# Kernel tuning notes

Measured on AMD Instinct MI355X. Metric: run time of the kernel, lower is better.

Reference implementation:

```python
import jax, jax.numpy as jnp
import numpy as np
import math

N, KZ, IFZ, AHZ, AFZ = 20000, 16, 256, 8, 32
EPS = 1e-5


def layernorm(x, g, b):
    m = jnp.mean(x, axis=-1, keepdims=True)
    v = jnp.mean((x - m) ** 2, axis=-1, keepdims=True)
    return (x - m) * jax.lax.rsqrt(v + EPS) * g + b


def rotate_half(x):
    x1, x2 = jnp.split(x, 2, axis=-1)
    return jnp.concatenate([-x2, x1], axis=-1)


def setup_inputs() -> dict:
    key = jax.random.key(0)
    ks = jax.random.split(key, 16)
    s = 1.0 / math.sqrt(IFZ)
    hf = AHZ * AFZ
    return {
        "x_1": jax.random.normal(ks[0], (N, IFZ), jnp.float32),
        "x_2": jax.random.normal(ks[1], (N, KZ, IFZ), jnp.float32),
        "pos_emb": jax.random.normal(ks[2], (N, AFZ), jnp.float32),
        "edge_index": jax.random.randint(ks[3], (N, KZ), 0, N),
        "Wq": jax.random.normal(ks[4], (IFZ, hf), jnp.float32) * s,
        "Wk": jax.random.normal(ks[5], (IFZ, hf), jnp.float32) * s,
        "Wv": jax.random.normal(ks[6], (IFZ, hf), jnp.float32) * s,
        "Wb": jax.random.normal(ks[7], (IFZ, AHZ), jnp.float32) * s,
        "bln_g": jnp.ones((IFZ,), jnp.float32),
        "bln_b": jnp.zeros((IFZ,), jnp.float32),
        "Wg": jax.random.normal(ks[8], (IFZ, hf), jnp.float32) * s,
        "bg": jnp.zeros((hf,), jnp.float32),
        "Wback": jax.random.normal(ks[9], (hf, IFZ), jnp.float32) / math.sqrt(hf),
        "bback": jnp.zeros((IFZ,), jnp.float32),
        "ln1_g": jnp.ones((IFZ,), jnp.float32),
        "ln1_b": jnp.zeros((IFZ,), jnp.float32),
    }


def reference(x_1, x_2, pos_emb, edge_index, Wq, Wk, Wv, Wb, bln_g, bln_b,
              Wg, bg, Wback, bback, ln1_g, ln1_b):
    n = x_1.shape[0]
    y_1 = x_1[edge_index]                                  # [N,kz,ifz] irregular gather
    q = (x_1 @ Wq).reshape(n, AHZ, AFZ)                    # [N,h,f]
    k = (y_1 @ Wk).reshape(n, KZ, AHZ, AFZ)                # [N,kz,h,f]
    # RoPE: rotate q by each node's own angles, k by gathered neighbor angles
    cos_q = jnp.cos(pos_emb)[:, None, :]                   # [N,1,f]
    sin_q = jnp.sin(pos_emb)[:, None, :]
    q = q * cos_q + rotate_half(q) * sin_q
    pe_n = pos_emb[edge_index]                             # [N,kz,f]
    cos_k = jnp.cos(pe_n)[:, :, None, :]                   # [N,kz,1,f]
    sin_k = jnp.sin(pe_n)[:, :, None, :]
    k = k * cos_k + rotate_half(k) * sin_k
    v = (y_1 @ Wv).reshape(n, KZ, AHZ, AFZ)
    bias_2 = layernorm(x_2, bln_g, bln_b) @ Wb             # [N,kz,h]
    gate = jax.nn.sigmoid(x_1 @ Wg + bg).reshape(n, AHZ, AFZ)
    scores = jnp.einsum('nhf,nkhf->nkh', q, k) / math.sqrt(AFZ) + bias_2
    w = jax.nn.softmax(scores, axis=1)                     # over kz neighbors
    out = gate * jnp.einsum('nkh,nkhf->nhf', w, v)         # [N,h,f]
    out = out.reshape(n, AHZ * AFZ) @ Wback + bback + math.sqrt(2.0) * x_1
    return layernorm(out, ln1_g, ln1_b)
```

## Files before the change

### kernel.cpp

```cpp
#include <hip/hip_runtime.h>
#include <math.h>

#define IFZ 256
#define KZ  16
#define AHZ 8
#define AFZ 32
#define HF  256

typedef _Float16 half8 __attribute__((ext_vector_type(8)));
typedef _Float16 half4 __attribute__((ext_vector_type(4)));
typedef float    f32x4 __attribute__((ext_vector_type(4)));

__global__ void prep_all(const float* __restrict__ w0, const float* __restrict__ w1,
                         const float* __restrict__ w2, const float* __restrict__ w3,
                         const float* __restrict__ w4, _Float16* __restrict__ out,
                         const float* __restrict__ g, const float* __restrict__ b,
                         const float* __restrict__ Wb,
                         _Float16* __restrict__ c1T, float* __restrict__ c23)
{
    const int m = blockIdx.y;
    if (m < 5) {
        int k = blockIdx.x;
        int c = threadIdx.x;
        const float* w = (m == 0) ? w0 : (m == 1) ? w1 : (m == 2) ? w2 : (m == 3) ? w3 : w4;
        out[(size_t)m * 65536 + (size_t)c * 256 + k] = (_Float16)w[(size_t)k * 256 + c];
        return;
    }
    if (blockIdx.x != 0) return;

    __shared__ float red[4][16];
    const int f = threadIdx.x;
    const int w = f >> 6, l = f & 63;
    const float gv = g[f], bv = b[f];
    float ph2[8], ph3[8];
    #pragma unroll
    for (int h = 0; h < 8; ++h) {
        float wv = Wb[(size_t)f * 8 + h];
        c1T[h * 256 + f] = (_Float16)(gv * wv);
        ph2[h] = gv * wv;
        ph3[h] = bv * wv;
    }
    c1T[8 * 256 + f] = (_Float16)1.0f;
    #pragma unroll
    for (int cc = 9; cc < 16; ++cc) c1T[cc * 256 + f] = (_Float16)0.0f;

    #pragma unroll
    for (int h = 0; h < 8; ++h) {
        #pragma unroll
        for (int o = 32; o > 0; o >>= 1) {
            ph2[h] += __shfl_xor(ph2[h], o);
            ph3[h] += __shfl_xor(ph3[h], o);
        }
        if (l == h) { red[w][h] = ph2[h]; red[w][8 + h] = ph3[h]; }
    }
    __syncthreads();
    if (f < 16) c23[f] = red[0][f] + red[1][f] + red[2][f] + red[3][f];
}

__launch_bounds__(256)
__global__ void gemm_qkvg(const float* __restrict__ A, const _Float16* __restrict__ WT,
                          const float* __restrict__ pe, const float* __restrict__ bg,
                          _Float16* __restrict__ QH, _Float16* __restrict__ KH,
                          _Float16* __restrict__ VH, _Float16* __restrict__ GH, int N)
{
    __shared__ _Float16 as[64][40];
    __shared__ _Float16 bs[4][64][40];

    const int tid = threadIdx.x;
    const int l   = tid & 63;
    const int w   = tid >> 6;
    const int n0  = blockIdx.x * 64;
    const int c0  = blockIdx.y * 64;

    f32x4 acc[4][4];
    #pragma unroll
    for (int m = 0; m < 4; ++m)
        #pragma unroll
        for (int b = 0; b < 4; ++b)
            { acc[m][b][0]=0.f; acc[m][b][1]=0.f; acc[m][b][2]=0.f; acc[m][b][3]=0.f; }

    const int srow = tid >> 2;
    const int sch  = (tid & 3) * 8;
    const size_t aoff = (size_t)(n0 + srow) * IFZ + sch;
    const size_t boff = (size_t)(c0 + srow) * IFZ + sch;
    const bool arow_ok = (n0 + srow < N);

    half8 av{}, bv0, bv1, bv2, bv3;
    if (arow_ok) {
        f32x4 a0 = *reinterpret_cast<const f32x4*>(A + aoff);
        f32x4 a1 = *reinterpret_cast<const f32x4*>(A + aoff + 4);
        av[0]=(_Float16)a0[0]; av[1]=(_Float16)a0[1]; av[2]=(_Float16)a0[2]; av[3]=(_Float16)a0[3];
        av[4]=(_Float16)a1[0]; av[5]=(_Float16)a1[1]; av[6]=(_Float16)a1[2]; av[7]=(_Float16)a1[3];
    }
    bv0 = *reinterpret_cast<const half8*>(WT + 0 * 65536 + boff);
    bv1 = *reinterpret_cast<const half8*>(WT + 1 * 65536 + boff);
    bv2 = *reinterpret_cast<const half8*>(WT + 2 * 65536 + boff);
    bv3 = *reinterpret_cast<const half8*>(WT + 3 * 65536 + boff);

    for (int kt = 0; kt < 8; ++kt) {
        __syncthreads();
        *reinterpret_cast<half8*>(&as[srow][sch])    = av;
        *reinterpret_cast<half8*>(&bs[0][srow][sch]) = bv0;
        *reinterpret_cast<half8*>(&bs[1][srow][sch]) = bv1;
        *reinterpret_cast<half8*>(&bs[2][srow][sch]) = bv2;
        *reinterpret_cast<half8*>(&bs[3][srow][sch]) = bv3;
        __syncthreads();

        half8 nav{}, nbv0{}, nbv1{}, nbv2{}, nbv3{};
        if (kt < 7) {
            const int k0 = (kt + 1) * 32;
            if (arow_ok) {
                f32x4 a0 = *reinterpret_cast<const f32x4*>(A + aoff + k0);
                f32x4 a1 = *reinterpret_cast<const f32x4*>(A + aoff + k0 + 4);
                nav[0]=(_Float16)a0[0]; nav[1]=(_Float16)a0[1]; nav[2]=(_Float16)a0[2]; nav[3]=(_Float16)a0[3];
                nav[4]=(_Float16)a1[0]; nav[5]=(_Float16)a1[1]; nav[6]=(_Float16)a1[2]; nav[7]=(_Float16)a1[3];
            }
            nbv0 = *reinterpret_cast<const half8*>(WT + 0 * 65536 + boff + k0);
            nbv1 = *reinterpret_cast<const half8*>(WT + 1 * 65536 + boff + k0);
            nbv2 = *reinterpret_cast<const half8*>(WT + 2 * 65536 + boff + k0);
            nbv3 = *reinterpret_cast<const half8*>(WT + 3 * 65536 + boff + k0);
        }

        half8 af = *reinterpret_cast<const half8*>(&as[16 * w + (l & 15)][8 * (l >> 4)]);
        #pragma unroll
        for (int m = 0; m < 4; ++m) {
            #pragma unroll
            for (int b = 0; b < 4; ++b) {
                half8 bf = *reinterpret_cast<const half8*>(&bs[m][16 * b + (l & 15)][8 * (l >> 4)]);
                acc[m][b] = __builtin_amdgcn_mfma_f32_16x16x32_f16(af, bf, acc[m][b], 0, 0, 0);
            }
        }
        av = nav; bv0 = nbv0; bv1 = nbv1; bv2 = nbv2; bv3 = nbv3;
    }

    #pragma unroll
    for (int r = 0; r < 4; ++r) {
        const int grow = n0 + 16 * w + ((l >> 4) << 2) + r;
        if (grow >= N) continue;
        float a0 = pe[(size_t)grow * AFZ + (l & 15)];
        float a1 = pe[(size_t)grow * AFZ + 16 + (l & 15)];
        float s0, c0f, s1, c1f;
        __sincosf(a0, &s0, &c0f);
        __sincosf(a1, &s1, &c1f);
        #pragma unroll
        for (int m = 0; m < 2; ++m) {
            _Float16* o = m ? KH : QH;
            #pragma unroll
            for (int pb = 0; pb < 4; pb += 2) {
                float v0 = acc[m][pb][r], v1 = acc[m][pb + 1][r];
                o[(size_t)grow * HF + c0 + 16 * pb       + (l & 15)] = (_Float16)(v0 * c0f - v1 * s0);
                o[(size_t)grow * HF + c0 + 16 * (pb + 1) + (l & 15)] = (_Float16)(v1 * c1f + v0 * s1);
            }
        }
        #pragma unroll
        for (int b = 0; b < 4; ++b)
            VH[(size_t)grow * HF + c0 + 16 * b + (l & 15)] = (_Float16)acc[2][b][r];
        #pragma unroll
        for (int b = 0; b < 4; ++b) {
            const int c = c0 + 16 * b + (l & 15);
            float v = acc[3][b][r] + bg[c];
            GH[(size_t)grow * HF + c] = (_Float16)(1.f / (1.f + __expf(-v)));
        }
    }
}

__launch_bounds__(256)
__global__ void attn_fused(const _Float16* __restrict__ Qh, const _Float16* __restrict__ Kh,
                           const _Float16* __restrict__ Vh, const _Float16* __restrict__ Gh,
                           const int* __restrict__ eidx, const float* __restrict__ x2,
                           const _Float16* __restrict__ c1T, const float* __restrict__ c23,
                           _Float16* __restrict__ AOh, int N)
{
    const int tid = threadIdx.x;
    const int l   = tid & 63;
    const int w   = tid >> 6;
    const int n   = blockIdx.x * 4 + w;
    if (n >= N) return;
    const int h = l >> 3;
    const int c = l & 15;
    const int p = l >> 4;

    const int ei_reg = eidx[(size_t)n * KZ + c];

    const float* xr = x2 + ((size_t)n * KZ + c) * IFZ + p * 8;
    f32x4 xv[16];
    #pragma unroll
    for (int kt = 0; kt < 8; ++kt) {
        xv[2 * kt]     = __builtin_nontemporal_load(reinterpret_cast<const f32x4*>(xr + kt * 32));
        xv[2 * kt + 1] = __builtin_nontemporal_load(reinterpret_cast<const f32x4*>(xr + kt * 32 + 4));
    }
    half8 bf[8];
    #pragma unroll
    for (int kt = 0; kt < 8; ++kt)
        bf[kt] = *reinterpret_cast<const half8*>(c1T + (size_t)c * 256 + kt * 32 + p * 8);

    f32x4 acc1 = {0.f, 0.f, 0.f, 0.f};
    f32x4 acc2 = {0.f, 0.f, 0.f, 0.f};
    #pragma unroll
    for (int kt = 0; kt < 8; ++kt) {
        f32x4 xa = xv[2 * kt], xb = xv[2 * kt + 1];
        half8 ax, ax2;
        ax[0] = (_Float16)xa[0]; ax[1] = (_Float16)xa[1];
        ax[2] = (_Float16)xa[2]; ax[3] = (_Float16)xa[3];
        ax[4] = (_Float16)xb[0]; ax[5] = (_Float16)xb[1];
        ax[6] = (_Float16)xb[2]; ax[7] = (_Float16)xb[3];
        ax2[0] = (_Float16)(xa[0] * xa[0]); ax2[1] = (_Float16)(xa[1] * xa[1]);
        ax2[2] = (_Float16)(xa[2] * xa[2]); ax2[3] = (_Float16)(xa[3] * xa[3]);
        ax2[4] = (_Float16)(xb[0] * xb[0]); ax2[5] = (_Float16)(xb[1] * xb[1]);
        ax2[6] = (_Float16)(xb[2] * xb[2]); ax2[7] = (_Float16)(xb[3] * xb[3]);
        acc1 = __builtin_amdgcn_mfma_f32_16x16x32_f16(ax,  bf[kt], acc1, 0, 0, 0);
        acc2 = __builtin_amdgcn_mfma_f32_16x16x32_f16(ax2, bf[kt], acc2, 0, 0, 0);
    }

    const float c2v = (c < 8) ? c23[c]     : 0.f;
    const float c3v = (c < 8) ? c23[8 + c] : 0.f;
    const int srcl = (l & 48) | 8;
    float bval[4];
    #pragma unroll
    for (int j = 0; j < 4; ++j) {
        float s1 = __shfl(acc1[j], srcl);
        float s2 = __shfl(acc2[j], srcl);
        float m    = s1 * (1.f / 256.f);
        float var  = s2 * (1.f / 256.f) - m * m;
        float rstd = rsqrtf(var + 1e-5f);
        bval[j] = rstd * (acc1[j] - m * c2v) + c3v;
    }

    half4 kreg[16];
    #pragma unroll
    for (int e = 0; e < 16; ++e) {
        const int row = __shfl(ei_reg, e);
        kreg[e] = *reinterpret_cast<const half4*>(Kh + (size_t)row * HF + 4 * l);
    }
    half4 vreg[16];
    #pragma unroll
    for (int e = 0; e < 16; ++e) {
        const int row = __shfl(ei_reg, e);
        vreg[e] = *reinterpret_cast<const half4*>(Vh + (size_t)row * HF + 4 * l);
    }

    half4 qh4 = *reinterpret_cast<const half4*>(Qh + (size_t)n * HF + 4 * l);
    const float q0 = (float)qh4[0], q1 = (float)qh4[1],
                q2 = (float)qh4[2], q3 = (float)qh4[3];

    float sc[16];
    #pragma unroll
    for (int e = 0; e < 16; ++e) {
        float s = q0 * (float)kreg[e][0] + q1 * (float)kreg[e][1]
                + q2 * (float)kreg[e][2] + q3 * (float)kreg[e][3];
        s += __shfl_xor(s, 1); s += __shfl_xor(s, 2); s += __shfl_xor(s, 4);
        sc[e] = s * 0.17677669529663687f
              + __shfl(bval[e & 3], ((e >> 2) << 4) | h);
    }

    float m = sc[0];
    #pragma unroll
    for (int e = 1; e < 16; ++e) m = fmaxf(m, sc[e]);
    float sum = 0.f;
    #pragma unroll
    for (int e = 0; e < 16; ++e) { sc[e] = __expf(sc[e] - m); sum += sc[e]; }
    const float inv = 1.f / sum;

    float o0 = 0.f, o1 = 0.f, o2 = 0.f, o3 = 0.f;
    #pragma unroll
    for (int e = 0; e < 16; ++e) {
        const float we = sc[e] * inv;
        o0 = fmaf(we, (float)vreg[e][0], o0);
        o1 = fmaf(we, (float)vreg[e][1], o1);
        o2 = fmaf(we, (float)vreg[e][2], o2);
        o3 = fmaf(we, (float)vreg[e][3], o3);
    }

    half4 gh4 = *reinterpret_cast<const half4*>(Gh + (size_t)n * HF + 4 * l);
    half4 oh;
    oh[0] = (_Float16)(o0 * (float)gh4[0]);
    oh[1] = (_Float16)(o1 * (float)gh4[1]);
    oh[2] = (_Float16)(o2 * (float)gh4[2]);
    oh[3] = (_Float16)(o3 * (float)gh4[3]);
    *reinterpret_cast<half4*>(AOh + (size_t)n * HF + 4 * l) = oh;
}

__launch_bounds__(256)
__global__ void gemm_back(const _Float16* __restrict__ A, const _Float16* __restrict__ BT,
                          const float* __restrict__ bias, float* __restrict__ Y, int N)
{
    __shared__ _Float16 as[64][40];
    __shared__ _Float16 bs[64][40];

    const int tid = threadIdx.x;
    const int l   = tid & 63;
    const int w   = tid >> 6;
    const int n0  = blockIdx.x * 64;
    const int c0  = blockIdx.y * 64;

    f32x4 acc[4];
    #pragma unroll
    for (int b = 0; b < 4; ++b) { acc[b][0]=0.f; acc[b][1]=0.f; acc[b][2]=0.f; acc[b][3]=0.f; }

    const int srow = tid >> 2;
    const int sch  = (tid & 3) * 8;
    const size_t aoff = (size_t)(n0 + srow) * IFZ + sch;
    const size_t boff = (size_t)(c0 + srow) * IFZ + sch;

    half8 av{}, bv;
    if (n0 + srow < N) av = *reinterpret_cast<const half8*>(A + aoff);
    bv = *reinterpret_cast<const half8*>(BT + boff);

    for (int kt = 0; kt < 8; ++kt) {
        __syncthreads();
        *reinterpret_cast<half8*>(&as[srow][sch]) = av;
        *reinterpret_cast<half8*>(&bs[srow][sch]) = bv;
        __syncthreads();

        half8 nav{}, nbv{};
        if (kt < 7) {
            const int k0 = (kt + 1) * 32;
            if (n0 + srow < N) nav = *reinterpret_cast<const half8*>(A + aoff + k0);
            nbv = *reinterpret_cast<const half8*>(BT + boff + k0);
        }

        half8 af = *reinterpret_cast<const half8*>(&as[16 * w + (l & 15)][8 * (l >> 4)]);
        #pragma unroll
        for (int b = 0; b < 4; ++b) {
            half8 bf = *reinterpret_cast<const half8*>(&bs[16 * b + (l & 15)][8 * (l >> 4)]);
            acc[b] = __builtin_amdgcn_mfma_f32_16x16x32_f16(af, bf, acc[b], 0, 0, 0);
        }
        av = nav; bv = nbv;
    }

    #pragma unroll
    for (int r = 0; r < 4; ++r) {
        const int grow = n0 + 16 * w + ((l >> 4) << 2) + r;
        if (grow >= N) continue;
        #pragma unroll
        for (int b = 0; b < 4; ++b) {
            const int c = c0 + 16 * b + (l & 15);
            Y[(size_t)grow * HF + c] = acc[b][r] + bias[c];
        }
    }
}

__launch_bounds__(256)
__global__ void final_ln(const float* __restrict__ RAWb,
                         const float* __restrict__ x1b,
                         const float* __restrict__ g1,
                         const float* __restrict__ b1,
                         float* __restrict__ outb,
                         int N)
{
    int n    = blockIdx.x * 4 + (threadIdx.x >> 6);
    int lane = threadIdx.x & 63;
    if (n >= N) return;
    const size_t off = (size_t)n * IFZ + lane * 4;
    float4 ur = *reinterpret_cast<const float4*>(RAWb + off);
    float4 ux = *reinterpret_cast<const float4*>(x1b + off);
    float x[4];
    x[0] = ur.x + 1.4142135623730951f * ux.x;
    x[1] = ur.y + 1.4142135623730951f * ux.y;
    x[2] = ur.z + 1.4142135623730951f * ux.z;
    x[3] = ur.w + 1.4142135623730951f * ux.w;
    float s = x[0] + x[1] + x[2] + x[3];
    float q = x[0]*x[0] + x[1]*x[1] + x[2]*x[2] + x[3]*x[3];
    #pragma unroll
    for (int o = 32; o > 0; o >>= 1) { s += __shfl_xor(s, o); q += __shfl_xor(q, o); }
    float m    = s * (1.f / 256.f);
    float var  = q * (1.f / 256.f) - m * m;
    float rstd = rsqrtf(var + 1e-5f);
    float4 uo;
    {
        int f = lane * 4;
        uo.x = (x[0] - m) * rstd * g1[f + 0] + b1[f + 0];
        uo.y = (x[1] - m) * rstd * g1[f + 1] + b1[f + 1];
        uo.z = (x[2] - m) * rstd * g1[f + 2] + b1[f + 2];
        uo.w = (x[3] - m) * rstd * g1[f + 3] + b1[f + 3];
    }
    *reinterpret_cast<float4*>(outb + off) = uo;
}

extern "C" void kernel_launch(void* const* d_in, const int* in_sizes, int n_in,
                              void* d_out, int out_size, void* d_ws, size_t ws_size,
                              hipStream_t stream)
{
    const float* x1   = (const float*)d_in[0];
    const float* x2   = (const float*)d_in[1];
    const float* pe   = (const float*)d_in[2];
    const int*   ei   = (const int*)d_in[3];
    const float* wq   = (const float*)d_in[4];
    const float* wk   = (const float*)d_in[5];
    const float* wv   = (const float*)d_in[6];
    const float* wb   = (const float*)d_in[7];
    const float* blng = (const float*)d_in[8];
    const float* blnb = (const float*)d_in[9];
    const float* wg   = (const float*)d_in[10];
    const float* bg   = (const float*)d_in[11];
    const float* wbk  = (const float*)d_in[12];
    const float* bbk  = (const float*)d_in[13];
    const float* g1   = (const float*)d_in[14];
    const float* b1   = (const float*)d_in[15];

    const int N = in_sizes[0] / IFZ;

    const size_t S2 = (((size_t)N * HF * 2) + 4095) & ~(size_t)4095;
    char* base = (char*)d_ws;
    _Float16* QH  = (_Float16*)(base);
    _Float16* KH  = (_Float16*)(base + 1 * S2);
    _Float16* VH  = (_Float16*)(base + 2 * S2);
    _Float16* GH  = (_Float16*)(base + 3 * S2);
    _Float16* WT  = (_Float16*)(base + 4 * S2);
    _Float16* C1T = (_Float16*)(base + 4 * S2 + (1u << 20));
    float*    C23 = (float*)   (base + 4 * S2 + (1u << 20) + 8192);
    _Float16* AOH = QH;
    float*    RAW = (float*)(base + 1 * S2);

    prep_all<<<dim3(256, 6), 256, 0, stream>>>(wq, wk, wv, wg, wbk, WT,
                                               blng, blnb, wb, C1T, C23);

    const int nt = (N + 63) / 64;
    gemm_qkvg<<<dim3(nt, 4), 256, 0, stream>>>(x1, WT, pe, bg, QH, KH, VH, GH, N);

    attn_fused<<<dim3((N + 3) / 4), 256, 0, stream>>>(QH, KH, VH, GH, ei, x2,
                                                      C1T, C23, AOH, N);

    gemm_back<<<dim3(nt, 4), 256, 0, stream>>>(AOH, WT + 4 * 65536, bbk, RAW, N);

    final_ln<<<dim3((N + 3) / 4), 256, 0, stream>>>(RAW, x1, g1, b1, (float*)d_out, N);
}
```

Measured before the change: 171.2 us.

## Move x_2 layernorm bias computation into QKVG GEMM launch as interleaved blocks

The streaming layernorm-bias computation over x_2 moves out of the attention kernel and into the QKVG GEMM launch as extra blocks, interleaved with the GEMM tiles through a proportional block mapping. The bias results go to a new B2 workspace buffer that the attention kernel reads back. This lets the bandwidth-heavy x_2 read overlap with the compute-bound GEMM and makes the attention kernel lighter. The cost is an extra write and read of an N*16*8 float buffer, plus a more complex block dispatch.

```diff
diff --git a/kernel.cpp b/kernel.cpp
--- a/kernel.cpp
+++ b/kernel.cpp
@@ -58,19 +58,85 @@
 }
 
 __launch_bounds__(256)
-__global__ void gemm_qkvg(const float* __restrict__ A, const _Float16* __restrict__ WT,
-                          const float* __restrict__ pe, const float* __restrict__ bg,
-                          _Float16* __restrict__ QH, _Float16* __restrict__ KH,
-                          _Float16* __restrict__ VH, _Float16* __restrict__ GH, int N)
+__global__ void qkvg_bias2(const float* __restrict__ A, const _Float16* __restrict__ WT,
+                           const float* __restrict__ pe, const float* __restrict__ bg,
+                           _Float16* __restrict__ QH, _Float16* __restrict__ KH,
+                           _Float16* __restrict__ VH, _Float16* __restrict__ GH,
+                           const float* __restrict__ x2, const _Float16* __restrict__ c1T,
+                           const float* __restrict__ c23, float* __restrict__ B2,
+                           int N, int R, int Aq, int grid)
 {
     __shared__ _Float16 as[64][40];
     __shared__ _Float16 bs[4][64][40];
+
+    const int bx  = blockIdx.x;
+    const long long t0 = (long long)bx * Aq / grid;
+    const long long t1 = (long long)(bx + 1) * Aq / grid;
+    const bool is_q = (t1 > t0);
 
     const int tid = threadIdx.x;
     const int l   = tid & 63;
     const int w   = tid >> 6;
-    const int n0  = blockIdx.x * 64;
-    const int c0  = blockIdx.y * 64;
+
+    if (!is_q) {
+        const int bidx = bx - (int)t0;
+        const int c = l & 15;
+        const int p = l >> 4;
+        const int R0 = (bidx * 4 + w) * 16;
+        if (R0 >= R) return;
+
+        const int arow = (R0 + c < R) ? (R0 + c) : (R - 1);
+        const float* xr = x2 + (size_t)arow * IFZ + p * 8;
+
+        f32x4 xv[16];
+        #pragma unroll
+        for (int kt = 0; kt < 8; ++kt) {
+            xv[2 * kt]     = __builtin_nontemporal_load(reinterpret_cast<const f32x4*>(xr + kt * 32));
+            xv[2 * kt + 1] = __builtin_nontemporal_load(reinterpret_cast<const f32x4*>(xr + kt * 32 + 4));
+        }
+        half8 bf[8];
+        #pragma unroll
+        for (int kt = 0; kt < 8; ++kt)
+            bf[kt] = *reinterpret_cast<const half8*>(c1T + (size_t)c * 256 + kt * 32 + p * 8);
+
+        f32x4 acc1 = {0.f, 0.f, 0.f, 0.f};
+        f32x4 acc2 = {0.f, 0.f, 0.f, 0.f};
+        #pragma unroll
+        for (int kt = 0; kt < 8; ++kt) {
+            f32x4 xa = xv[2 * kt], xb = xv[2 * kt + 1];
+            half8 ax, ax2;
+            ax[0] = (_Float16)xa[0]; ax[1] = (_Float16)xa[1];
+            ax[2] = (_Float16)xa[2]; ax[3] = (_Float16)xa[3];
+            ax[4] = (_Float16)xb[0]; ax[5] = (_Float16)xb[1];
+            ax[6] = (_Float16)xb[2]; ax[7] = (_Float16)xb[3];
+            ax2[0] = (_Float16)(xa[0] * xa[0]); ax2[1] = (_Float16)(xa[1] * xa[1]);
+            ax2[2] = (_Float16)(xa[2] * xa[2]); ax2[3] = (_Float16)(xa[3] * xa[3]);
+            ax2[4] = (_Float16)(xb[0] * xb[0]); ax2[5] = (_Float16)(xb[1] * xb[1]);
+            ax2[6] = (_Float16)(xb[2] * xb[2]); ax2[7] = (_Float16)(xb[3] * xb[3]);
+            acc1 = __builtin_amdgcn_mfma_f32_16x16x32_f16(ax,  bf[kt], acc1, 0, 0, 0);
+            acc2 = __builtin_amdgcn_mfma_f32_16x16x32_f16(ax2, bf[kt], acc2, 0, 0, 0);
+        }
+
+        const float c2v = (c < 8) ? c23[c]     : 0.f;
+        const float c3v = (c < 8) ? c23[8 + c] : 0.f;
+        const int srcl = (l & 48) | 8;
+        #pragma unroll
+        for (int j = 0; j < 4; ++j) {
+            float s1 = __shfl(acc1[j], srcl);
+            float s2 = __shfl(acc2[j], srcl);
+            float m    = s1 * (1.f / 256.f);
+            float var  = s2 * (1.f / 256.f) - m * m;
+            float rstd = rsqrtf(var + 1e-5f);
+            const int row = R0 + 4 * p + j;
+            if (c < 8 && row < R)
+                B2[(size_t)row * 8 + c] = rstd * (acc1[j] - m * c2v) + c3v;
+        }
+        return;
+    }
+
+    const int tile = (int)t0;
+    const int n0   = (tile >> 2) * 64;
+    const int c0   = (tile & 3) * 64;
 
     f32x4 acc[4][4];
     #pragma unroll
@@ -126,8 +192,8 @@
         for (int m = 0; m < 4; ++m) {
             #pragma unroll
             for (int b = 0; b < 4; ++b) {
-                half8 bf = *reinterpret_cast<const half8*>(&bs[m][16 * b + (l & 15)][8 * (l >> 4)]);
-                acc[m][b] = __builtin_amdgcn_mfma_f32_16x16x32_f16(af, bf, acc[m][b], 0, 0, 0);
+                half8 bfm = *reinterpret_cast<const half8*>(&bs[m][16 * b + (l & 15)][8 * (l >> 4)]);
+                acc[m][b] = __builtin_amdgcn_mfma_f32_16x16x32_f16(af, bfm, acc[m][b], 0, 0, 0);
             }
         }
         av = nav; bv0 = nbv0; bv1 = nbv1; bv2 = nbv2; bv3 = nbv3;
@@ -165,11 +231,10 @@
 }
 
 __launch_bounds__(256)
-__global__ void attn_fused(const _Float16* __restrict__ Qh, const _Float16* __restrict__ Kh,
-                           const _Float16* __restrict__ Vh, const _Float16* __restrict__ Gh,
-                           const int* __restrict__ eidx, const float* __restrict__ x2,
-                           const _Float16* __restrict__ c1T, const float* __restrict__ c23,
-                           _Float16* __restrict__ AOh, int N)
+__global__ void attn_node(const _Float16* __restrict__ Qh, const _Float16* __restrict__ Kh,
+                          const _Float16* __restrict__ Vh, const _Float16* __restrict__ Gh,
+                          const int* __restrict__ eidx, const float* __restrict__ b2,
+                          _Float16* __restrict__ AOh, int N)
 {
     const int tid = threadIdx.x;
     const int l   = tid & 63;
@@ -177,54 +242,11 @@
     const int n   = blockIdx.x * 4 + w;
     if (n >= N) return;
     const int h = l >> 3;
-    const int c = l & 15;
-    const int p = l >> 4;
-
-    const int ei_reg = eidx[(size_t)n * KZ + c];
-
-    const float* xr = x2 + ((size_t)n * KZ + c) * IFZ + p * 8;
-    f32x4 xv[16];
-    #pragma unroll
-    for (int kt = 0; kt < 8; ++kt) {
-        xv[2 * kt]     = __builtin_nontemporal_load(reinterpret_cast<const f32x4*>(xr + kt * 32));
-        xv[2 * kt + 1] = __builtin_nontemporal_load(reinterpret_cast<const f32x4*>(xr + kt * 32 + 4));
-    }
-    half8 bf[8];
-    #pragma unroll
-    for (int kt = 0; kt < 8; ++kt)
-        bf[kt] = *reinterpret_cast<const half8*>(c1T + (size_t)c * 256 + kt * 32 + p * 8);
-
-    f32x4 acc1 = {0.f, 0.f, 0.f, 0.f};
-    f32x4 acc2 = {0.f, 0.f, 0.f, 0.f};
-    #pragma unroll
-    for (int kt = 0; kt < 8; ++kt) {
-        f32x4 xa = xv[2 * kt], xb = xv[2 * kt + 1];
-        half8 ax, ax2;
-        ax[0] = (_Float16)xa[0]; ax[1] = (_Float16)xa[1];
-        ax[2] = (_Float16)xa[2]; ax[3] = (_Float16)xa[3];
-        ax[4] = (_Float16)xb[0]; ax[5] = (_Float16)xb[1];
-        ax[6] = (_Float16)xb[2]; ax[7] = (_Float16)xb[3];
-        ax2[0] = (_Float16)(xa[0] * xa[0]); ax2[1] = (_Float16)(xa[1] * xa[1]);
-        ax2[2] = (_Float16)(xa[2] * xa[2]); ax2[3] = (_Float16)(xa[3] * xa[3]);
-        ax2[4] = (_Float16)(xb[0] * xb[0]); ax2[5] = (_Float16)(xb[1] * xb[1]);
-        ax2[6] = (_Float16)(xb[2] * xb[2]); ax2[7] = (_Float16)(xb[3] * xb[3]);
-        acc1 = __builtin_amdgcn_mfma_f32_16x16x32_f16(ax,  bf[kt], acc1, 0, 0, 0);
-        acc2 = __builtin_amdgcn_mfma_f32_16x16x32_f16(ax2, bf[kt], acc2, 0, 0, 0);
-    }
-
-    const float c2v = (c < 8) ? c23[c]     : 0.f;
-    const float c3v = (c < 8) ? c23[8 + c] : 0.f;
-    const int srcl = (l & 48) | 8;
-    float bval[4];
-    #pragma unroll
-    for (int j = 0; j < 4; ++j) {
-        float s1 = __shfl(acc1[j], srcl);
-        float s2 = __shfl(acc2[j], srcl);
-        float m    = s1 * (1.f / 256.f);
-        float var  = s2 * (1.f / 256.f) - m * m;
-        float rstd = rsqrtf(var + 1e-5f);
-        bval[j] = rstd * (acc1[j] - m * c2v) + c3v;
-    }
+
+    const int ei_reg = eidx[(size_t)n * KZ + (l & 15)];
+
+    const float b2a = b2[(size_t)n * 128 + l];
+    const float b2b = b2[(size_t)n * 128 + 64 + l];
 
     half4 kreg[16];
     #pragma unroll
@@ -249,9 +271,12 @@
         float s = q0 * (float)kreg[e][0] + q1 * (float)kreg[e][1]
                 + q2 * (float)kreg[e][2] + q3 * (float)kreg[e][3];
         s += __shfl_xor(s, 1); s += __shfl_xor(s, 2); s += __shfl_xor(s, 4);
-        sc[e] = s * 0.17677669529663687f
-              + __shfl(bval[e & 3], ((e >> 2) << 4) | h);
-    }
+        sc[e] = s * 0.17677669529663687f;
+    }
+    #pragma unroll
+    for (int e = 0; e < 8; ++e) sc[e]     += __shfl(b2a, e * 8 + h);
+    #pragma unroll
+    for (int e = 0; e < 8; ++e) sc[e + 8] += __shfl(b2b, e * 8 + h);
 
     float m = sc[0];
     #pragma unroll
@@ -399,6 +424,7 @@
     const float* b1   = (const float*)d_in[15];
 
     const int N = in_sizes[0] / IFZ;
+    const int R = N * KZ;
 
     const size_t S2 = (((size_t)N * HF * 2) + 4095) & ~(size_t)4095;
     char* base = (char*)d_ws;
@@ -409,6 +435,7 @@
     _Float16* WT  = (_Float16*)(base + 4 * S2);
     _Float16* C1T = (_Float16*)(base + 4 * S2 + (1u << 20));
     float*    C23 = (float*)   (base + 4 * S2 + (1u << 20) + 8192);
+    float*    B2  = (float*)   (base + 4 * S2 + (2u << 20));
     _Float16* AOH = QH;
     float*    RAW = (float*)(base + 1 * S2);
 
@@ -416,10 +443,13 @@
                                                blng, blnb, wb, C1T, C23);
 
     const int nt = (N + 63) / 64;
-    gemm_qkvg<<<dim3(nt, 4), 256, 0, stream>>>(x1, WT, pe, bg, QH, KH, VH, GH, N);
-
-    attn_fused<<<dim3((N + 3) / 4), 256, 0, stream>>>(QH, KH, VH, GH, ei, x2,
-                                                      C1T, C23, AOH, N);
+    const int Aq = nt * 4;
+    const int Rb = (R + 63) / 64;
+    const int grid = Aq + Rb;
+    qkvg_bias2<<<dim3(grid), 256, 0, stream>>>(x1, WT, pe, bg, QH, KH, VH, GH,
+                                               x2, C1T, C23, B2, N, R, Aq, grid);
+
+    attn_node<<<dim3((N + 3) / 4), 256, 0, stream>>>(QH, KH, VH, GH, ei, B2, AOH, N);
 
     gemm_back<<<dim3(nt, 4), 256, 0, stream>>>(AOH, WT + 4 * 65536, bbk, RAW, N);
 
```

Measured after the change: 191.5 us. +11.9%, slower.
